# Kernel tuning notes

Measured on AMD Instinct MI355X. Metric: run time of the kernel, lower is better.

Reference implementation:

```python
import jax, jax.numpy as jnp
import numpy as np
from jax import lax

SCORE_THRESHOLD = 0.001
IOU_THRESHOLD = 0.7
MAX_DETECTIONS = 300
PRE_NMS_TOPK = 1024      # standard pre-NMS candidate cap (torchvision/YOLO practice)
CLASS_OFFSET = 4096.0    # > max image coord, separates classes so cross-class IoU == 0
IMG = 640.0

B, N, C = 32, 8400, 80


def setup_inputs() -> dict:
    key = jax.random.key(0)
    kc, ks, kp = jax.random.split(key, 3)
    # well-formed boxes in [y1, x1, y2, x2] convention (matches repo's nms())
    tl = jax.random.uniform(kc, (B, N, 2), jnp.float32, 0.0, IMG - 1.0)   # (y1, x1)
    wh = jax.random.uniform(ks, (B, N, 2), jnp.float32, 4.0, 160.0)      # (h, w)
    boxes = jnp.concatenate([tl, jnp.minimum(tl + wh, IMG)], axis=-1)     # [B,N,4]
    scores = jax.random.uniform(kp, (B, N, C), jnp.float32)               # [B,N,C]
    return {"boxes": boxes, "scores": scores}


def _pairwise_iou(b):
    # b: [B,K,4] as [y1,x1,y2,x2]; +1 pixel convention per the repo's nms()
    y1, x1, y2, x2 = b[..., 0], b[..., 1], b[..., 2], b[..., 3]
    areas = (x2 - x1 + 1.0) * (y2 - y1 + 1.0)                             # [B,K]
    yy1 = jnp.maximum(y1[:, :, None], y1[:, None, :])
    xx1 = jnp.maximum(x1[:, :, None], x1[:, None, :])
    yy2 = jnp.minimum(y2[:, :, None], y2[:, None, :])
    xx2 = jnp.minimum(x2[:, :, None], x2[:, None, :])
    w = jnp.maximum(0.0, xx2 - xx1 + 1.0)
    h = jnp.maximum(0.0, yy2 - yy1 + 1.0)
    inter = w * h                                                          # [B,K,K]
    return inter / (areas[:, :, None] + areas[:, None, :] - inter)


def multiclass_nms(boxes, scores):
    b, n, c = scores.shape
    flat = jnp.where(scores > SCORE_THRESHOLD, scores, 0.0).reshape(b, n * c)
    top_scores, top_idx = lax.top_k(flat, PRE_NMS_TOPK)                    # [B,K]
    box_idx = top_idx // c
    cls_idx = top_idx % c                                                  # int32 [B,K]
    cand = jnp.take_along_axis(boxes, box_idx[..., None], axis=1)          # [B,K,4]
    # offset boxes by class so per-class NMS happens in one shared pass
    off = cand + (cls_idx.astype(cand.dtype) * CLASS_OFFSET)[..., None]
    iou = _pairwise_iou(off)                                               # [B,K,K]

    k = PRE_NMS_TOPK
    idx = jnp.arange(k)
    keep0 = top_scores > SCORE_THRESHOLD                                   # [B,K]

    def body(i, keep):
        row = iou[:, i, :]                                                 # [B,K]
        sup = (row > IOU_THRESHOLD) & keep[:, i][:, None] & (idx[None, :] > i)
        return keep & ~sup

    keep = lax.fori_loop(0, k, body, keep0)                                # greedy NMS

    final_scores = jnp.where(keep, top_scores, 0.0)
    out_scores, sel = lax.top_k(final_scores, MAX_DETECTIONS)              # [B,300]
    out_boxes = jnp.take_along_axis(cand, sel[..., None], axis=1)          # [B,300,4]
    out_labels = jnp.take_along_axis(cls_idx, sel, axis=1)                 # [B,300]
    n_valid = jnp.minimum(jnp.sum(keep, axis=1, keepdims=True), MAX_DETECTIONS)
    return out_boxes, out_scores, out_labels.astype(jnp.int32), n_valid.astype(jnp.int32)


def reference(boxes, scores):
    return multiclass_nms(boxes, scores)
```

## Files before the change

kernel.cpp:

```cpp
#include <hip/hip_runtime.h>
#include <cstdint>
#include <cstddef>

#define B_      32
#define N_      8400
#define C_      80
#define NC      672000
#define NCV4    168000
#define NBINS   4096
#define TOPK    1024
#define MAXDET  300
#define CANDCAP 4096
#define NSLICE  16
#define SLICE_V4 10500
#define SEGCAP  256

#define STAGE_THRESH 0.998046875f

#define WS_CANDKEYS  0
#define WS_SEGCNT    1048576
#define WS_TOPSCORE  1050624
#define WS_TOPBOX    1181696
#define WS_TOPCLS    1705984
#define WS_KEEP      1837056

#define OUT_SCORES  38400
#define OUT_LABELS  48000
#define OUT_NVALID  57600

__global__ __launch_bounds__(256) void stage_kernel(const float4* __restrict__ scores4,
                                                    unsigned* __restrict__ segCnt,
                                                    unsigned long long* __restrict__ candKeys) {
    __shared__ unsigned lcnt;
    int b = blockIdx.x, sl = blockIdx.y, tid = threadIdx.x;
    if (tid == 0) lcnt = 0;
    __syncthreads();
    const float4* s = scores4 + (size_t)b * NCV4 + (size_t)sl * SLICE_V4;
    unsigned long long* seg = candKeys + (size_t)b * CANDCAP + (size_t)sl * SEGCAP;
    for (int i = tid; i < SLICE_V4; i += 256) {
        float4 v = s[i];
        float c[4] = {v.x, v.y, v.z, v.w};
        unsigned flat0 = ((unsigned)sl * SLICE_V4 + (unsigned)i) * 4u;
        #pragma unroll
        for (int kc = 0; kc < 4; ++kc) {
            float x = (c[kc] > 0.001f) ? c[kc] : 0.0f;
            if (x >= STAGE_THRESH) {
                unsigned p = atomicAdd(&lcnt, 1u);
                if (p < (unsigned)SEGCAP)
                    seg[p] = ((unsigned long long)__float_as_uint(x) << 32) |
                             (unsigned long long)(0xFFFFFFFFu - (flat0 + kc));
            }
        }
    }
    __syncthreads();
    if (tid == 0) segCnt[b * NSLICE + sl] = lcnt;
}

__global__ __launch_bounds__(1024) void sort_gather_kernel(
        const float4* __restrict__ scores4,
        const unsigned long long* __restrict__ candKeys,
        const unsigned* __restrict__ segCnt,
        const float* __restrict__ boxes,
        float* __restrict__ topScore,
        float* __restrict__ topBox,
        int* __restrict__ topCls) {
    __shared__ union {
        unsigned long long k[CANDCAP];
        unsigned fh[2 * CANDCAP];
    } u;
    __shared__ unsigned pref[NSLICE + 1];
    __shared__ int s_fb;
    __shared__ unsigned scnt;
    __shared__ int s_cut;
    int b = blockIdx.x;
    int tid = threadIdx.x;

    if (tid < NSLICE) pref[tid + 1] = segCnt[b * NSLICE + tid];
    __syncthreads();
    if (tid == 0) {
        unsigned acc = 0; int fb2 = 0;
        pref[0] = 0;
        for (int s2 = 1; s2 <= NSLICE; ++s2) {
            unsigned c2 = pref[s2];
            if (c2 > (unsigned)SEGCAP) fb2 = 1;
            acc += c2;
            pref[s2] = acc;
        }
        if (acc < (unsigned)TOPK || acc > (unsigned)CANDCAP) fb2 = 1;
        s_fb = fb2;
    }
    __syncthreads();

    unsigned M;
    if (!s_fb) {
        int w = tid >> 6, lane = tid & 63;
        unsigned base2 = pref[w], n2 = pref[w + 1] - base2;
        const unsigned long long* src =
            candKeys + (size_t)b * CANDCAP + (size_t)w * SEGCAP;
        for (unsigned t = lane; t < n2; t += 64) u.k[base2 + t] = src[t];
        M = pref[NSLICE];
    } else {
        for (int i2 = tid; i2 < NBINS; i2 += 1024) u.fh[i2] = 0;
        if (tid == 0) scnt = 0;
        __syncthreads();
        const float4* s = scores4 + (size_t)b * NCV4;
        for (int i2 = tid; i2 < NCV4; i2 += 1024) {
            float4 v = s[i2];
            float c4[4] = {v.x, v.y, v.z, v.w};
            #pragma unroll
            for (int kc = 0; kc < 4; ++kc) {
                float x = (c4[kc] > 0.001f) ? c4[kc] : 0.0f;
                int bin = (int)(x * 4096.0f);
                bin = bin > (NBINS - 1) ? (NBINS - 1) : bin;
                atomicAdd(&u.fh[bin], 1u);
            }
        }
        __syncthreads();
        if (tid == 0) {
            unsigned acc = 0; int cb = 0;
            for (int bin = NBINS - 1; bin >= 0; --bin) {
                acc += u.fh[bin];
                if (acc >= (unsigned)TOPK) { cb = bin; break; }
            }
            s_cut = cb;
        }
        __syncthreads();
        int cb = s_cut;
        for (int i2 = tid; i2 < NCV4; i2 += 1024) {
            float4 v = s[i2];
            float c4[4] = {v.x, v.y, v.z, v.w};
            unsigned flat0 = (unsigned)i2 * 4u;
            #pragma unroll
            for (int kc = 0; kc < 4; ++kc) {
                float x = (c4[kc] > 0.001f) ? c4[kc] : 0.0f;
                int bin = (int)(x * 4096.0f);
                bin = bin > (NBINS - 1) ? (NBINS - 1) : bin;
                if (bin >= cb) {
                    unsigned p = atomicAdd(&scnt, 1u);
                    if (p < (unsigned)CANDCAP)
                        u.k[p] = ((unsigned long long)__float_as_uint(x) << 32) |
                                 (unsigned long long)(0xFFFFFFFFu - (flat0 + kc));
                }
            }
        }
        __syncthreads();
        M = scnt;
        if (M > (unsigned)CANDCAP) M = CANDCAP;
    }
    int S = (M <= 1024u) ? 1024 : (M <= 2048u ? 2048 : CANDCAP);
    for (int i2 = tid; i2 < S; i2 += 1024)
        if (i2 >= (int)M) u.k[i2] = 0ull;
    __syncthreads();

    for (int kk = 2; kk <= S; kk <<= 1) {
        for (int j = kk >> 1; j > 0; j >>= 1) {
            if (j >= 32) __syncthreads();
            else         __threadfence_block();
            for (int t = tid; t < S; t += 1024) {
                int l = t ^ j;
                if (l > t) {
                    unsigned long long a0 = u.k[t], c0 = u.k[l];
                    bool sw = ((t & kk) == 0) ? (a0 < c0) : (a0 > c0);
                    if (sw) { u.k[t] = c0; u.k[l] = a0; }
                }
            }
        }
    }
    __syncthreads();

    int i = tid;
    unsigned long long key = u.k[i];
    float sc = __uint_as_float((unsigned)(key >> 32));
    unsigned idx = 0xFFFFFFFFu - (unsigned)(key & 0xFFFFFFFFull);
    if (idx >= (unsigned)NC) idx = 0;
    unsigned bi = idx / (unsigned)C_;
    unsigned cl = idx - bi * (unsigned)C_;
    const float* bp = boxes + (size_t)b * N_ * 4 + (size_t)bi * 4;
    float c0 = bp[0], c1 = bp[1], c2 = bp[2], c3 = bp[3];
    topScore[b * TOPK + i] = sc;
    float* tb = topBox + ((size_t)b * TOPK + i) * 4;
    tb[0] = c0; tb[1] = c1; tb[2] = c2; tb[3] = c3;
    topCls[b * TOPK + i] = (int)cl;
}

#define CLS_CAP 256
__global__ __launch_bounds__(64) void nms_kernel(const float* __restrict__ topScore,
                                                 const float* __restrict__ topBox,
                                                 const int* __restrict__ topCls,
                                                 int* __restrict__ keep) {
    __shared__ unsigned short pos[CLS_CAP];
    __shared__ float by1[CLS_CAP], bx1[CLS_CAP], by2[CLS_CAP], bx2[CLS_CAP];
    __shared__ float barea[CLS_CAP];
    __shared__ unsigned char sup[CLS_CAP];
    int b = blockIdx.x;
    int c = blockIdx.y;
    int lane = threadIdx.x;
    const float* ts = topScore + b * TOPK;
    const int*   tc = topCls + b * TOPK;
    int*         kp = keep + b * TOPK;
    float off = (float)c * 4096.0f;
    int base = 0;
    for (int chunkS = 0; chunkS < TOPK; chunkS += 64) {
        int i = chunkS + lane;
        int cls = tc[i];
        float sc = ts[i];
        bool mine = (cls == c);
        bool listed = mine && (sc > 0.001f);
        if (mine) kp[i] = 0;
        unsigned long long mask = __ballot(listed);
        int rank = __popcll(mask & ((1ull << lane) - 1ull));
        if (listed) {
            int slot = base + rank;
            if (slot < CLS_CAP) {
                pos[slot] = (unsigned short)i;
                const float* tb = topBox + ((size_t)(b * TOPK + i)) * 4;
                float y1 = tb[0] + off, x1 = tb[1] + off;
                float y2 = tb[2] + off, x2 = tb[3] + off;
                by1[slot] = y1; bx1[slot] = x1; by2[slot] = y2; bx2[slot] = x2;
                barea[slot] = __fmul_rn((x2 - x1) + 1.0f, (y2 - y1) + 1.0f);
                sup[slot] = 0;
            }
        }
        base += __popcll(mask);
    }
    int m = base < CLS_CAP ? base : CLS_CAP;
    __syncthreads();
    int cur = 0;
    while (cur < m) {
        if (lane == 0) kp[pos[cur]] = 1;
        float cy1 = by1[cur], cx1 = bx1[cur], cy2 = by2[cur], cx2 = bx2[cur];
        float carea = barea[cur];
        for (int j = cur + 1 + lane; j < m; j += 64) {
            if (!sup[j]) {
                float yy1 = fmaxf(cy1, by1[j]), xx1 = fmaxf(cx1, bx1[j]);
                float yy2 = fminf(cy2, by2[j]), xx2 = fminf(cx2, bx2[j]);
                float w = fmaxf(0.0f, (xx2 - xx1) + 1.0f);
                float h = fmaxf(0.0f, (yy2 - yy1) + 1.0f);
                float inter = __fmul_rn(w, h);
                float denom = (carea + barea[j]) - inter;
                float iou = inter / denom;
                if (iou > 0.7f) sup[j] = 1;
            }
        }
        __syncthreads();
        int nxt = m;
        for (int j = cur + 1 + lane; j < m; j += 64)
            if (!sup[j]) { nxt = j; break; }
        for (int o = 32; o > 0; o >>= 1) {
            int other = __shfl_xor(nxt, o, 64);
            nxt = nxt < other ? nxt : other;
        }
        cur = nxt;
    }
}

__global__ __launch_bounds__(1024) void finalize_kernel(const float* __restrict__ topScore,
                                                        const float* __restrict__ topBox,
                                                        const int* __restrict__ topCls,
                                                        const int* __restrict__ keep,
                                                        float* __restrict__ out) {
    __shared__ int sk[TOPK];
    __shared__ int sel[MAXDET];
    int b = blockIdx.x;
    int i = threadIdx.x;
    int kp = keep[b * TOPK + i];
    sk[i] = kp;
    __syncthreads();
    for (int off = 1; off < TOPK; off <<= 1) {
        int add = (i >= off) ? sk[i - off] : 0;
        __syncthreads();
        sk[i] += add;
        __syncthreads();
    }
    int nk = sk[TOPK - 1];
    int incl = sk[i];
    int kexcl = incl - kp;
    int sexcl = i - kexcl;
    if (kp) {
        if (kexcl < MAXDET) sel[kexcl] = i;
    } else {
        int slot = nk + sexcl;
        if (slot < MAXDET) sel[slot] = i;
    }
    __syncthreads();
    if (i < MAXDET) {
        int p = sel[i];
        float sc = (i < nk) ? topScore[b * TOPK + p] : 0.0f;
        const float* tb = topBox + ((size_t)b * TOPK + p) * 4;
        float* ob = out + ((size_t)b * MAXDET + i) * 4;
        ob[0] = tb[0]; ob[1] = tb[1]; ob[2] = tb[2]; ob[3] = tb[3];
        out[OUT_SCORES + b * MAXDET + i] = sc;
        out[OUT_LABELS + b * MAXDET + i] = (float)topCls[b * TOPK + p];
    }
    if (i == 0) out[OUT_NVALID + b] = (float)(nk < MAXDET ? nk : MAXDET);
}

extern "C" void kernel_launch(void* const* d_in, const int* in_sizes, int n_in,
                              void* d_out, int out_size, void* d_ws, size_t ws_size,
                              hipStream_t stream) {
    const float* boxes  = (const float*)d_in[0];
    const float* scores = (const float*)d_in[1];
    float* out = (float*)d_out;
    char* ws = (char*)d_ws;

    unsigned long long* candKeys = (unsigned long long*)(ws + WS_CANDKEYS);
    unsigned* segCnt = (unsigned*)(ws + WS_SEGCNT);
    float* topScore = (float*)(ws + WS_TOPSCORE);
    float* topBox = (float*)(ws + WS_TOPBOX);
    int* topCls = (int*)(ws + WS_TOPCLS);
    int* keep = (int*)(ws + WS_KEEP);

    const float4* scores4 = (const float4*)scores;

    stage_kernel<<<dim3(B_, NSLICE), 256, 0, stream>>>(scores4, segCnt, candKeys);
    sort_gather_kernel<<<B_, 1024, 0, stream>>>(scores4, candKeys, segCnt, boxes,
                                                topScore, topBox, topCls);
    nms_kernel<<<dim3(B_, C_), 64, 0, stream>>>(topScore, topBox, topCls, keep);
    finalize_kernel<<<B_, 1024, 0, stream>>>(topScore, topBox, topCls, keep, out);
}
```

Measured before the change: 198.6 us.

## Bucket staged candidates by score bin and sort each bucket in separate small blocks

The stage kernel now scatters candidates into 8 score buckets per slice, each with its own small per-slice region. A new 64-thread kernel, launched per (batch, bucket), merges its bucket and bitonic-sorts at most 256 keys. It writes its slice of the top-K directly at an offset given by the counts of the higher buckets, and buckets that fall entirely past the top-K exit early. This replaces one 1024-thread block per batch sorting up to 4096 keys with many small independent sorts. The histogram path moves to a separate fallback kernel that exits early unless a per-batch flag is set, which costs one extra launch.

```diff
diff --git a/kernel.cpp b/kernel.cpp
--- a/kernel.cpp
+++ b/kernel.cpp
@@ -13,16 +13,19 @@
 #define CANDCAP 4096
 #define NSLICE  16
 #define SLICE_V4 10500
-#define SEGCAP  256
+#define NBKT    8
+#define SEGB    64
+#define BSORT   256
 
 #define STAGE_THRESH 0.998046875f
 
-#define WS_CANDKEYS  0
-#define WS_SEGCNT    1048576
-#define WS_TOPSCORE  1050624
-#define WS_TOPBOX    1181696
-#define WS_TOPCLS    1705984
-#define WS_KEEP      1837056
+#define WS_SEGKEYS  0
+#define WS_SEGCNT   2097152
+#define WS_FBFLAG   2113536
+#define WS_TOPSCORE 2113664
+#define WS_TOPBOX   2244736
+#define WS_TOPCLS   2769024
+#define WS_KEEP     2900096
 
 #define OUT_SCORES  38400
 #define OUT_LABELS  48000
@@ -30,13 +33,12 @@
 
 __global__ __launch_bounds__(256) void stage_kernel(const float4* __restrict__ scores4,
                                                     unsigned* __restrict__ segCnt,
-                                                    unsigned long long* __restrict__ candKeys) {
-    __shared__ unsigned lcnt;
+                                                    unsigned long long* __restrict__ segKeys) {
+    __shared__ unsigned lcnt[NBKT];
     int b = blockIdx.x, sl = blockIdx.y, tid = threadIdx.x;
-    if (tid == 0) lcnt = 0;
+    if (tid < NBKT) lcnt[tid] = 0;
     __syncthreads();
     const float4* s = scores4 + (size_t)b * NCV4 + (size_t)sl * SLICE_V4;
-    unsigned long long* seg = candKeys + (size_t)b * CANDCAP + (size_t)sl * SEGCAP;
     for (int i = tid; i < SLICE_V4; i += 256) {
         float4 v = s[i];
         float c[4] = {v.x, v.y, v.z, v.w};
@@ -45,117 +47,169 @@
         for (int kc = 0; kc < 4; ++kc) {
             float x = (c[kc] > 0.001f) ? c[kc] : 0.0f;
             if (x >= STAGE_THRESH) {
-                unsigned p = atomicAdd(&lcnt, 1u);
-                if (p < (unsigned)SEGCAP)
-                    seg[p] = ((unsigned long long)__float_as_uint(x) << 32) |
-                             (unsigned long long)(0xFFFFFFFFu - (flat0 + kc));
-            }
-        }
-    }
-    __syncthreads();
-    if (tid == 0) segCnt[b * NSLICE + sl] = lcnt;
-}
-
-__global__ __launch_bounds__(1024) void sort_gather_kernel(
+                int bin = (int)(x * 4096.0f);
+                bin = bin > (NBINS - 1) ? (NBINS - 1) : bin;
+                int bkt = bin - 4088;
+                unsigned p = atomicAdd(&lcnt[bkt], 1u);
+                if (p < (unsigned)SEGB)
+                    segKeys[(((size_t)(b * NBKT + bkt)) * NSLICE + sl) * SEGB + p] =
+                        ((unsigned long long)__float_as_uint(x) << 32) |
+                        (unsigned long long)(0xFFFFFFFFu - (flat0 + kc));
+            }
+        }
+    }
+    __syncthreads();
+    if (tid < NBKT) segCnt[(b * NBKT + tid) * NSLICE + sl] = lcnt[tid];
+}
+
+__global__ __launch_bounds__(64) void sortb_kernel(
+        const unsigned long long* __restrict__ segKeys,
+        const unsigned* __restrict__ segCnt,
+        const float4* __restrict__ boxes4,
+        unsigned* __restrict__ fbFlag,
+        float* __restrict__ topScore,
+        float4* __restrict__ topBox4,
+        int* __restrict__ topCls) {
+    __shared__ unsigned long long k[BSORT];
+    __shared__ unsigned bsum[NBKT];
+    __shared__ unsigned bok[NBKT];
+    __shared__ unsigned spref[NSLICE + 1];
+    int b = blockIdx.x, bkt = blockIdx.y, lane = threadIdx.x;
+
+    if (lane < NBKT) {
+        const unsigned* c = segCnt + (b * NBKT + lane) * NSLICE;
+        unsigned ssum = 0, ok = 1;
+        for (int sl = 0; sl < NSLICE; ++sl) {
+            unsigned v = c[sl];
+            if (v > (unsigned)SEGB) ok = 0;
+            ssum += v;
+        }
+        bsum[lane] = ssum; bok[lane] = ok;
+    }
+    __threadfence_block();
+    unsigned M = 0, base = 0; int valid = 1;
+    #pragma unroll
+    for (int t = 0; t < NBKT; ++t) {
+        unsigned s2 = bsum[t];
+        if (!bok[t] || s2 > (unsigned)BSORT) valid = 0;
+        M += s2;
+        if (t > bkt) base += s2;
+    }
+    unsigned n = bsum[bkt];
+    if (M < (unsigned)TOPK || M > (unsigned)CANDCAP) valid = 0;
+    if (bkt == 0 && lane == 0) fbFlag[b] = valid ? 0u : 1u;
+    if (!valid || base >= (unsigned)TOPK || n == 0) return;
+
+    if (lane == 0) {
+        unsigned acc = 0; spref[0] = 0;
+        const unsigned* c = segCnt + (b * NBKT + bkt) * NSLICE;
+        for (int sl = 0; sl < NSLICE; ++sl) { acc += c[sl]; spref[sl + 1] = acc; }
+    }
+    __threadfence_block();
+    for (int sl = 0; sl < NSLICE; ++sl) {
+        unsigned b0 = spref[sl], c2 = spref[sl + 1] - b0;
+        const unsigned long long* src =
+            segKeys + (((size_t)(b * NBKT + bkt)) * NSLICE + sl) * SEGB;
+        for (unsigned t = lane; t < c2; t += 64) k[b0 + t] = src[t];
+    }
+    for (unsigned t = n + lane; t < (unsigned)BSORT; t += 64) k[t] = 0ull;
+    __threadfence_block();
+
+    for (int kk = 2; kk <= BSORT; kk <<= 1) {
+        for (int j = kk >> 1; j > 0; j >>= 1) {
+            for (int c2 = lane; c2 < BSORT / 2; c2 += 64) {
+                int t = ((c2 & ~(j - 1)) << 1) | (c2 & (j - 1));
+                int l = t | j;
+                unsigned long long a0 = k[t], c0 = k[l];
+                bool sw = ((t & kk) == 0) ? (a0 < c0) : (a0 > c0);
+                if (sw) { k[t] = c0; k[l] = a0; }
+            }
+            __threadfence_block();
+        }
+    }
+
+    unsigned wlim = (unsigned)TOPK - base; if (wlim > n) wlim = n;
+    for (unsigned r = lane; r < wlim; r += 64) {
+        unsigned long long key = k[r];
+        float sc = __uint_as_float((unsigned)(key >> 32));
+        unsigned idx = 0xFFFFFFFFu - (unsigned)(key & 0xFFFFFFFFull);
+        if (idx >= (unsigned)NC) idx = 0;
+        unsigned bi = idx / (unsigned)C_;
+        unsigned cl = idx - bi * (unsigned)C_;
+        unsigned pos = base + r;
+        topScore[b * TOPK + pos] = sc;
+        topBox4[b * TOPK + pos] = boxes4[(size_t)b * N_ + bi];
+        topCls[b * TOPK + pos] = (int)cl;
+    }
+}
+
+__global__ __launch_bounds__(1024) void fallback_kernel(
         const float4* __restrict__ scores4,
-        const unsigned long long* __restrict__ candKeys,
-        const unsigned* __restrict__ segCnt,
+        const unsigned* __restrict__ fbFlag,
         const float* __restrict__ boxes,
         float* __restrict__ topScore,
         float* __restrict__ topBox,
         int* __restrict__ topCls) {
+    int b = blockIdx.x;
+    if (fbFlag[b] == 0) return;
     __shared__ union {
         unsigned long long k[CANDCAP];
-        unsigned fh[2 * CANDCAP];
+        unsigned fh[NBINS];
     } u;
-    __shared__ unsigned pref[NSLICE + 1];
-    __shared__ int s_fb;
     __shared__ unsigned scnt;
     __shared__ int s_cut;
-    int b = blockIdx.x;
     int tid = threadIdx.x;
-
-    if (tid < NSLICE) pref[tid + 1] = segCnt[b * NSLICE + tid];
+    for (int i2 = tid; i2 < NBINS; i2 += 1024) u.fh[i2] = 0;
+    if (tid == 0) scnt = 0;
+    __syncthreads();
+    const float4* s = scores4 + (size_t)b * NCV4;
+    for (int i2 = tid; i2 < NCV4; i2 += 1024) {
+        float4 v = s[i2];
+        float c4[4] = {v.x, v.y, v.z, v.w};
+        #pragma unroll
+        for (int kc = 0; kc < 4; ++kc) {
+            float x = (c4[kc] > 0.001f) ? c4[kc] : 0.0f;
+            int bin = (int)(x * 4096.0f);
+            bin = bin > (NBINS - 1) ? (NBINS - 1) : bin;
+            atomicAdd(&u.fh[bin], 1u);
+        }
+    }
     __syncthreads();
     if (tid == 0) {
-        unsigned acc = 0; int fb2 = 0;
-        pref[0] = 0;
-        for (int s2 = 1; s2 <= NSLICE; ++s2) {
-            unsigned c2 = pref[s2];
-            if (c2 > (unsigned)SEGCAP) fb2 = 1;
-            acc += c2;
-            pref[s2] = acc;
-        }
-        if (acc < (unsigned)TOPK || acc > (unsigned)CANDCAP) fb2 = 1;
-        s_fb = fb2;
-    }
-    __syncthreads();
-
-    unsigned M;
-    if (!s_fb) {
-        int w = tid >> 6, lane = tid & 63;
-        unsigned base2 = pref[w], n2 = pref[w + 1] - base2;
-        const unsigned long long* src =
-            candKeys + (size_t)b * CANDCAP + (size_t)w * SEGCAP;
-        for (unsigned t = lane; t < n2; t += 64) u.k[base2 + t] = src[t];
-        M = pref[NSLICE];
-    } else {
-        for (int i2 = tid; i2 < NBINS; i2 += 1024) u.fh[i2] = 0;
-        if (tid == 0) scnt = 0;
-        __syncthreads();
-        const float4* s = scores4 + (size_t)b * NCV4;
-        for (int i2 = tid; i2 < NCV4; i2 += 1024) {
-            float4 v = s[i2];
-            float c4[4] = {v.x, v.y, v.z, v.w};
-            #pragma unroll
-            for (int kc = 0; kc < 4; ++kc) {
-                float x = (c4[kc] > 0.001f) ? c4[kc] : 0.0f;
-                int bin = (int)(x * 4096.0f);
-                bin = bin > (NBINS - 1) ? (NBINS - 1) : bin;
-                atomicAdd(&u.fh[bin], 1u);
-            }
-        }
-        __syncthreads();
-        if (tid == 0) {
-            unsigned acc = 0; int cb = 0;
-            for (int bin = NBINS - 1; bin >= 0; --bin) {
-                acc += u.fh[bin];
-                if (acc >= (unsigned)TOPK) { cb = bin; break; }
-            }
-            s_cut = cb;
-        }
-        __syncthreads();
-        int cb = s_cut;
-        for (int i2 = tid; i2 < NCV4; i2 += 1024) {
-            float4 v = s[i2];
-            float c4[4] = {v.x, v.y, v.z, v.w};
-            unsigned flat0 = (unsigned)i2 * 4u;
-            #pragma unroll
-            for (int kc = 0; kc < 4; ++kc) {
-                float x = (c4[kc] > 0.001f) ? c4[kc] : 0.0f;
-                int bin = (int)(x * 4096.0f);
-                bin = bin > (NBINS - 1) ? (NBINS - 1) : bin;
-                if (bin >= cb) {
-                    unsigned p = atomicAdd(&scnt, 1u);
-                    if (p < (unsigned)CANDCAP)
-                        u.k[p] = ((unsigned long long)__float_as_uint(x) << 32) |
-                                 (unsigned long long)(0xFFFFFFFFu - (flat0 + kc));
-                }
-            }
-        }
-        __syncthreads();
-        M = scnt;
-        if (M > (unsigned)CANDCAP) M = CANDCAP;
-    }
+        unsigned acc = 0; int cb = 0;
+        for (int bin = NBINS - 1; bin >= 0; --bin) {
+            acc += u.fh[bin];
+            if (acc >= (unsigned)TOPK) { cb = bin; break; }
+        }
+        s_cut = cb;
+    }
+    __syncthreads();
+    int cb = s_cut;
+    for (int i2 = tid; i2 < NCV4; i2 += 1024) {
+        float4 v = s[i2];
+        float c4[4] = {v.x, v.y, v.z, v.w};
+        unsigned flat0 = (unsigned)i2 * 4u;
+        #pragma unroll
+        for (int kc = 0; kc < 4; ++kc) {
+            float x = (c4[kc] > 0.001f) ? c4[kc] : 0.0f;
+            int bin = (int)(x * 4096.0f);
+            bin = bin > (NBINS - 1) ? (NBINS - 1) : bin;
+            if (bin >= cb) {
+                unsigned p = atomicAdd(&scnt, 1u);
+                if (p < (unsigned)CANDCAP)
+                    u.k[p] = ((unsigned long long)__float_as_uint(x) << 32) |
+                             (unsigned long long)(0xFFFFFFFFu - (flat0 + kc));
+            }
+        }
+    }
+    __syncthreads();
+    unsigned M = scnt; if (M > (unsigned)CANDCAP) M = CANDCAP;
     int S = (M <= 1024u) ? 1024 : (M <= 2048u ? 2048 : CANDCAP);
     for (int i2 = tid; i2 < S; i2 += 1024)
         if (i2 >= (int)M) u.k[i2] = 0ull;
     __syncthreads();
-
     for (int kk = 2; kk <= S; kk <<= 1) {
         for (int j = kk >> 1; j > 0; j >>= 1) {
-            if (j >= 32) __syncthreads();
-            else         __threadfence_block();
             for (int t = tid; t < S; t += 1024) {
                 int l = t ^ j;
                 if (l > t) {
@@ -164,12 +218,10 @@
                     if (sw) { u.k[t] = c0; u.k[l] = a0; }
                 }
             }
-        }
-    }
-    __syncthreads();
-
-    int i = tid;
-    unsigned long long key = u.k[i];
+            __syncthreads();
+        }
+    }
+    unsigned long long key = u.k[tid];
     float sc = __uint_as_float((unsigned)(key >> 32));
     unsigned idx = 0xFFFFFFFFu - (unsigned)(key & 0xFFFFFFFFull);
     if (idx >= (unsigned)NC) idx = 0;
@@ -177,10 +229,10 @@
     unsigned cl = idx - bi * (unsigned)C_;
     const float* bp = boxes + (size_t)b * N_ * 4 + (size_t)bi * 4;
     float c0 = bp[0], c1 = bp[1], c2 = bp[2], c3 = bp[3];
-    topScore[b * TOPK + i] = sc;
-    float* tb = topBox + ((size_t)b * TOPK + i) * 4;
+    topScore[b * TOPK + tid] = sc;
+    float* tb = topBox + ((size_t)b * TOPK + tid) * 4;
     tb[0] = c0; tb[1] = c1; tb[2] = c2; tb[3] = c3;
-    topCls[b * TOPK + i] = (int)cl;
+    topCls[b * TOPK + tid] = (int)cl;
 }
 
 #define CLS_CAP 256
@@ -303,18 +355,22 @@
     float* out = (float*)d_out;
     char* ws = (char*)d_ws;
 
-    unsigned long long* candKeys = (unsigned long long*)(ws + WS_CANDKEYS);
+    unsigned long long* segKeys = (unsigned long long*)(ws + WS_SEGKEYS);
     unsigned* segCnt = (unsigned*)(ws + WS_SEGCNT);
+    unsigned* fbFlag = (unsigned*)(ws + WS_FBFLAG);
     float* topScore = (float*)(ws + WS_TOPSCORE);
     float* topBox = (float*)(ws + WS_TOPBOX);
     int* topCls = (int*)(ws + WS_TOPCLS);
     int* keep = (int*)(ws + WS_KEEP);
 
     const float4* scores4 = (const float4*)scores;
-
-    stage_kernel<<<dim3(B_, NSLICE), 256, 0, stream>>>(scores4, segCnt, candKeys);
-    sort_gather_kernel<<<B_, 1024, 0, stream>>>(scores4, candKeys, segCnt, boxes,
-                                                topScore, topBox, topCls);
+    const float4* boxes4  = (const float4*)boxes;
+
+    stage_kernel<<<dim3(B_, NSLICE), 256, 0, stream>>>(scores4, segCnt, segKeys);
+    sortb_kernel<<<dim3(B_, NBKT), 64, 0, stream>>>(segKeys, segCnt, boxes4, fbFlag,
+                                                    topScore, (float4*)topBox, topCls);
+    fallback_kernel<<<B_, 1024, 0, stream>>>(scores4, fbFlag, boxes,
+                                             topScore, topBox, topCls);
     nms_kernel<<<dim3(B_, C_), 64, 0, stream>>>(topScore, topBox, topCls, keep);
     finalize_kernel<<<B_, 1024, 0, stream>>>(topScore, topBox, topCls, keep, out);
 }
```

New measurement: 190.5 us. 4.1% less time.
